# Optimization experiments

Hardware: AMD Instinct MI355X
Metric: run time of the kernel (lower is better)

## Reference

```python
import jax, jax.numpy as jnp
import numpy as np

N_NODES = 100000
N_EDGES = 3200000
D_IN = 256
D_HID = 97


def setup_inputs() -> dict:
    key = jax.random.key(0)
    k1, k2, k3, k4, k5, k6 = jax.random.split(key, 6)
    x = jax.random.normal(k1, (N_NODES, D_IN), dtype=jnp.float32)
    edge_index = jax.random.randint(k2, (2, N_EDGES), 0, N_NODES, dtype=jnp.int64)
    # GCNConv weights (stored as [in, out]) and biases
    W1 = jax.random.normal(k3, (D_IN, D_HID), dtype=jnp.float32) / np.sqrt(D_IN)
    b1 = jnp.zeros((D_HID,), dtype=jnp.float32)
    W2 = jax.random.normal(k4, (D_HID, D_HID), dtype=jnp.float32) / np.sqrt(D_HID)
    b2 = jnp.zeros((D_HID,), dtype=jnp.float32)
    return {"x": x, "edge_index": edge_index, "W1": W1, "b1": b1, "W2": W2, "b2": b2}


def reference(x, edge_index, W1, b1, W2, b2):
    # PyG GCNConv: add self-loops, symmetric degree normalization,
    # out[i] = sum_j norm_ij * (x[j] @ W) + b
    N = x.shape[0]
    self_idx = jnp.arange(N, dtype=edge_index.dtype)
    src = jnp.concatenate([edge_index[0], self_idx])  # source j
    dst = jnp.concatenate([edge_index[1], self_idx])  # target i
    deg = jax.ops.segment_sum(jnp.ones_like(dst, dtype=x.dtype), dst, num_segments=N)
    dinv = jnp.where(deg > 0, 1.0 / jnp.sqrt(deg), 0.0)
    norm = dinv[src] * dinv[dst]  # [E+N]

    def gcn(h, W, b):
        h = h @ W  # dense linear transform first (out_dim small)
        msg = h[src] * norm[:, None]  # gather + scale
        agg = jax.ops.segment_sum(msg, dst, num_segments=N)  # scatter-add
        return agg + b

    h = jax.nn.relu(gcn(x, W1, b1))
    out = gcn(h, W2, b2)
    return out
```

## Files before the change

kernel.cpp:

```cpp
#include <hip/hip_runtime.h>
#include <hip/hip_fp16.h>
#include <stdint.h>

#define D_IN 256
#define D_H  97
#define RST  96
#define NPB  512
#define NBMAX 256
#define CHUNK 4096

typedef _Float16 f16;
typedef f16   f16x8 __attribute__((ext_vector_type(8)));
typedef float f32x4 __attribute__((ext_vector_type(4)));

__device__ __forceinline__ int load_idx(const void* p, int is64, long long pos) {
  if (is64) return (int)(((const long long*)p)[pos]);
  return ((const int*)p)[pos];
}

__global__ __launch_bounds__(256) void detect_prep(
    const void* ei, long long E, int* flag, int* __restrict__ bcur, int nbuck,
    const float* __restrict__ W1, const float* __restrict__ b1,
    const float* __restrict__ W2, const float* __restrict__ b2,
    f16* __restrict__ W1lin, f16* __restrict__ W2lin,
    float* __restrict__ b1p, float* __restrict__ b2p) {
  int tid = threadIdx.x;
  if (blockIdx.x == 0) {
    const int* p32 = (const int*)ei;
    long long stride = E / 1024; if (stride < 1) stride = 1;
    for (int i = tid; i <= nbuck; i += 256) bcur[i] = 0;
    int bad = 0;
    for (int s = 0; s < 4; ++s) {
      long long k = ((long long)tid * 4 + s) * stride;
      if (k < E) {
        if (p32[2 * k + 1] != 0) bad = 1;
      }
    }
    __shared__ int sh_bad;
    if (tid == 0) sh_bad = 0;
    __syncthreads();
    if (bad) atomicOr(&sh_bad, 1);
    __syncthreads();
    if (tid == 0) *flag = sh_bad ? 0 : 1;
    return;
  }
  int idx = (blockIdx.x - 1) * 256 + tid;
  const int n1 = 8 * 7 * 512;
  const int n2 = 4 * 7 * 512;
  if (idx < n1) {
    int fid = idx >> 3, hh = idx & 7;
    int lane = fid & 63, fg = fid >> 6;
    int kb = fg / 7, cg = fg % 7;
    int c = cg * 16 + (lane & 15);
    int k = kb * 32 + (lane >> 4) * 8 + hh;
    W1lin[idx] = (f16)((c < D_H && k < 256) ? W1[k * D_H + c] : 0.f);
  } else if (idx < n1 + n2) {
    int j = idx - n1;
    int fid = j >> 3, hh = j & 7;
    int lane = fid & 63, fg = fid >> 6;
    int kb = fg / 7, cg = fg % 7;
    int c = cg * 16 + (lane & 15);
    int k = kb * 32 + (lane >> 4) * 8 + hh;
    W2lin[j] = (f16)((c < D_H && k < D_H) ? W2[k * D_H + c] : 0.f);
  } else if (idx < n1 + n2 + 128) {
    int c = idx - (n1 + n2);
    b1p[c] = (c < D_H) ? b1[c] : 0.0f;
  } else if (idx < n1 + n2 + 256) {
    int c = idx - (n1 + n2 + 128);
    b2p[c] = (c < D_H) ? b2[c] : 0.0f;
  }
}

template<int KI, bool IN_HALF, bool SCALE_DINV>
__device__ __forceinline__ void gemm_body(
    int gb, const float* __restrict__ Af, const f16* __restrict__ Ah,
    const __half2* __restrict__ sideA,
    const f16* __restrict__ Wlin, const float* __restrict__ dinv,
    f16* __restrict__ C, __half2* __restrict__ sideC, int N) {
  int tid = threadIdx.x, wave = tid >> 6, lane = tid & 63;
  int row0 = gb * 128;
  int m = lane & 15, q = lane >> 4;
  int kf = q * 8;
  int r0 = row0 + wave * 32 + m;
  int r1 = r0 + 16;
  int rr0 = (r0 < N) ? r0 : 0;
  int rr1 = (r1 < N) ? r1 : 0;
  const f16* wbase = Wlin + lane * 8;

  f16x8 a0[KI], a1[KI];
  #pragma unroll
  for (int kb = 0; kb < KI; ++kb) {
    if constexpr (!IN_HALF) {
      const float* p0 = &Af[(size_t)rr0 * 256 + kb * 32 + kf];
      const float* p1 = &Af[(size_t)rr1 * 256 + kb * 32 + kf];
      float4 u0 = *(const float4*)p0, u1 = *(const float4*)(p0 + 4);
      float4 w0 = *(const float4*)p1, w1 = *(const float4*)(p1 + 4);
      f16x8 t0, t1;
      t0[0] = (f16)u0.x; t0[1] = (f16)u0.y; t0[2] = (f16)u0.z; t0[3] = (f16)u0.w;
      t0[4] = (f16)u1.x; t0[5] = (f16)u1.y; t0[6] = (f16)u1.z; t0[7] = (f16)u1.w;
      t1[0] = (f16)w0.x; t1[1] = (f16)w0.y; t1[2] = (f16)w0.z; t1[3] = (f16)w0.w;
      t1[4] = (f16)w1.x; t1[5] = (f16)w1.y; t1[6] = (f16)w1.z; t1[7] = (f16)w1.w;
      a0[kb] = t0; a1[kb] = t1;
    } else {
      if (kb < KI - 1) {
        a0[kb] = *(const f16x8*)&Ah[(size_t)rr0 * RST + kb * 32 + kf];
        a1[kb] = *(const f16x8*)&Ah[(size_t)rr1 * RST + kb * 32 + kf];
      } else {
        f16x8 z0, z1;
        #pragma unroll
        for (int j = 0; j < 8; ++j) { z0[j] = (f16)0.f; z1[j] = (f16)0.f; }
        if (q == 0) {
          z0[0] = ((const f16*)sideA)[2 * rr0];
          z1[0] = ((const f16*)sideA)[2 * rr1];
        }
        a0[kb] = z0; a1[kb] = z1;
      }
    }
  }

  f32x4 acc[2][7];
  #pragma unroll
  for (int mg = 0; mg < 2; ++mg)
    #pragma unroll
    for (int cg = 0; cg < 7; ++cg)
      #pragma unroll
      for (int j = 0; j < 4; ++j) acc[mg][cg][j] = 0.f;

  #pragma unroll
  for (int kb = 0; kb < KI; ++kb) {
    #pragma unroll
    for (int cg = 0; cg < 7; ++cg) {
      f16x8 b = *(const f16x8*)&wbase[(kb * 7 + cg) * 512];
      acc[0][cg] = __builtin_amdgcn_mfma_f32_16x16x32_f16(a0[kb], b, acc[0][cg], 0, 0, 0);
      acc[1][cg] = __builtin_amdgcn_mfma_f32_16x16x32_f16(a1[kb], b, acc[1][cg], 0, 0, 0);
    }
  }

  int colb = m, rq = q * 4;
  #pragma unroll
  for (int mg = 0; mg < 2; ++mg) {
    #pragma unroll
    for (int j = 0; j < 4; ++j) {
      int r = row0 + wave * 32 + mg * 16 + rq + j;
      if (r >= N) continue;
      float dv = SCALE_DINV ? dinv[r] : 1.0f;
      #pragma unroll
      for (int cg = 0; cg < 7; ++cg) {
        int c = cg * 16 + colb;
        float val = SCALE_DINV ? (acc[mg][cg][j] * dv) : acc[mg][cg][j];
        if (c < 96)       C[(size_t)r * RST + c] = (f16)val;
        else if (c == 96) sideC[r] = __floats2half2_rn(val, 0.f);
      }
    }
  }
}

__global__ __launch_bounds__(256) void scatter_gemm1(
    const void* ei, const int* __restrict__ flag, int* __restrict__ bcur,
    unsigned int* __restrict__ bsd, long long E, int nbuck, int cap, int nScat,
    const float* __restrict__ x, const f16* __restrict__ W1lin,
    f16* __restrict__ t1, __half2* __restrict__ sideT, int N) {
  __shared__ unsigned int packs[CHUNK];
  __shared__ unsigned char bkts[CHUNK];
  __shared__ int hist[NBMAX];
  __shared__ int gpos[NBMAX];
  __shared__ int cur[NBMAX];
  int tid = threadIdx.x;
  if ((int)blockIdx.x >= nScat) {
    gemm_body<8, false, false>(blockIdx.x - nScat, x, nullptr, nullptr,
                               W1lin, nullptr, t1, sideT, N);
    return;
  }
  if (tid < NBMAX) { hist[tid] = 0; cur[tid] = 0; }
  __syncthreads();
  int f = *flag;
  long long base = (long long)blockIdx.x * CHUNK;
  int cnt = (int)((E - base < CHUNK) ? (E - base) : CHUNK);
  #pragma unroll 4
  for (int i = tid; i < cnt; i += 256) {
    long long e = base + i;
    int s = load_idx(ei, f, e);
    int d = load_idx(ei, f, E + e);
    int b = d >> 9;
    packs[i] = ((unsigned int)(d & (NPB - 1)) << 17) | (unsigned int)s;
    bkts[i] = (unsigned char)b;
    atomicAdd(&hist[b], 1);
  }
  __syncthreads();
  if (tid < nbuck) { int h = hist[tid]; if (h) gpos[tid] = atomicAdd(&bcur[tid], h); }
  __syncthreads();
  #pragma unroll 4
  for (int i = tid; i < cnt; i += 256) {
    int b = bkts[i];
    int r = atomicAdd(&cur[b], 1);
    int idx = gpos[b] + r;
    if (idx < cap) bsd[(size_t)b * cap + idx] = packs[i];
  }
}

__global__ __launch_bounds__(256) void bucket_finalize(
    const unsigned int* __restrict__ bsd, const int* __restrict__ bcur,
    int* __restrict__ row_start, float* __restrict__ dinv,
    int* __restrict__ csr_src, int N, int cap, int nbuck) {
  __shared__ int sc[256];
  __shared__ int h[NPB];
  __shared__ int rs[NPB];
  __shared__ int cur[NPB];
  __shared__ int wsum[4];
  int b = blockIdx.x, tid = threadIdx.x;
  int lane = tid & 63, wid = tid >> 6;
  int v = (tid < nbuck) ? min(bcur[tid], cap) : 0;
  sc[tid] = v;
  h[2 * tid] = 0; h[2 * tid + 1] = 0;
  cur[2 * tid] = 0; cur[2 * tid + 1] = 0;
  __syncthreads();
  for (int o = 1; o < 256; o <<= 1) {
    int a = (tid >= o) ? sc[tid - o] : 0;
    __syncthreads();
    sc[tid] += a;
    __syncthreads();
  }
  int cnt = min(bcur[b], cap);
  int base = sc[b] - cnt;
  if (b == 0 && tid == 0) row_start[N] = sc[255];
  int d0 = b * cap;
  for (int i = tid; i < cnt; i += 256) atomicAdd(&h[bsd[d0 + i] >> 17], 1);
  __syncthreads();
  int a0 = h[2 * tid], a1 = h[2 * tid + 1];
  int tsum = a0 + a1;
  int incl = tsum;
  #pragma unroll
  for (int off = 1; off < 64; off <<= 1) {
    int n = __shfl_up(incl, off, 64);
    if (lane >= off) incl += n;
  }
  if (lane == 63) wsum[wid] = incl;
  __syncthreads();
  int woff = 0;
  for (int k = 0; k < wid; ++k) woff += wsum[k];
  int excl = woff + incl - tsum + base;
  rs[2 * tid] = excl;
  rs[2 * tid + 1] = excl + a0;
  int node0 = b * NPB;
  int n0 = node0 + 2 * tid, n1 = node0 + 2 * tid + 1;
  if (n0 < N) { row_start[n0] = excl;      dinv[n0] = rsqrtf((float)(a0 + 1)); }
  if (n1 < N) { row_start[n1] = excl + a0; dinv[n1] = rsqrtf((float)(a1 + 1)); }
  __syncthreads();
  for (int i = tid; i < cnt; i += 256) {
    unsigned int p = bsd[d0 + i];
    int r = p >> 17;
    int s = (int)(p & 0x1FFFFu);
    int rel = atomicAdd(&cur[r], 1);
    csr_src[rs[r] + rel] = s;
  }
}

__global__ __launch_bounds__(256) void mfma_gemm2(
    const f16* __restrict__ Ah, const __half2* __restrict__ sideA,
    const f16* __restrict__ Wlin, const float* __restrict__ dinv,
    f16* __restrict__ C, __half2* __restrict__ sideC, int N) {
  gemm_body<4, true, true>(blockIdx.x, nullptr, Ah, sideA, Wlin, dinv, C, sideC, N);
}

template<bool OUT_HALF, bool DO_RELU, bool SRC_SCALE>
__global__ __launch_bounds__(256) void agg_kernel(
    const __half* __restrict__ t, const __half2* __restrict__ side,
    const int* __restrict__ csr_src, const int* __restrict__ row_start,
    const float* __restrict__ dinv, const float* __restrict__ bias,
    void* __restrict__ outp, __half2* __restrict__ side_out, int N) {
  int lane = threadIdx.x & 63;
  int node = blockIdx.x * (blockDim.x >> 6) + (threadIdx.x >> 6);
  if (node >= N || lane >= 49) return;
  const char* gbase = (lane < 48) ? (const char*)t + lane * 4 : (const char*)side;
  unsigned gscale = (lane < 48) ? (unsigned)(RST * 2) : 4u;
  auto GATHER = [&](int j) -> float2 {
    return __half22float2(*(const __half2*)(gbase + (size_t)((unsigned)j * gscale)));
  };
  int s = row_start[node], epd = row_start[node + 1];
  float di = dinv[node];
  float2 v = GATHER(node);
  float ax, ay;
  if (SRC_SCALE) { ax = di * v.x; ay = di * v.y; }
  else           { ax = v.x;      ay = v.y; }
  int e = s;
  while ((e & 3) && e < epd) {
    int j = csr_src[e];
    float2 u = GATHER(j);
    if (SRC_SCALE) { float w = dinv[j]; ax = fmaf(w, u.x, ax); ay = fmaf(w, u.y, ay); }
    else           { ax += u.x; ay += u.y; }
    ++e;
  }
  for (; e + 8 <= epd; e += 8) {
    int4 q0 = *(const int4*)(csr_src + e);
    int4 q1 = *(const int4*)(csr_src + e + 4);
    float2 u0 = GATHER(q0.x), u1 = GATHER(q0.y), u2 = GATHER(q0.z), u3 = GATHER(q0.w);
    float2 u4 = GATHER(q1.x), u5 = GATHER(q1.y), u6 = GATHER(q1.z), u7 = GATHER(q1.w);
    if (SRC_SCALE) {
      float w0 = dinv[q0.x], w1 = dinv[q0.y], w2 = dinv[q0.z], w3 = dinv[q0.w];
      float w4 = dinv[q1.x], w5 = dinv[q1.y], w6 = dinv[q1.z], w7 = dinv[q1.w];
      ax += (fmaf(w0, u0.x, w1 * u1.x) + fmaf(w2, u2.x, w3 * u3.x)) +
            (fmaf(w4, u4.x, w5 * u5.x) + fmaf(w6, u6.x, w7 * u7.x));
      ay += (fmaf(w0, u0.y, w1 * u1.y) + fmaf(w2, u2.y, w3 * u3.y)) +
            (fmaf(w4, u4.y, w5 * u5.y) + fmaf(w6, u6.y, w7 * u7.y));
    } else {
      ax += ((u0.x + u1.x) + (u2.x + u3.x)) + ((u4.x + u5.x) + (u6.x + u7.x));
      ay += ((u0.y + u1.y) + (u2.y + u3.y)) + ((u4.y + u5.y) + (u6.y + u7.y));
    }
  }
  if (e + 4 <= epd) {
    int4 q0 = *(const int4*)(csr_src + e);
    float2 u0 = GATHER(q0.x), u1 = GATHER(q0.y), u2 = GATHER(q0.z), u3 = GATHER(q0.w);
    if (SRC_SCALE) {
      float w0 = dinv[q0.x], w1 = dinv[q0.y], w2 = dinv[q0.z], w3 = dinv[q0.w];
      ax += fmaf(w0, u0.x, w1 * u1.x) + fmaf(w2, u2.x, w3 * u3.x);
      ay += fmaf(w0, u0.y, w1 * u1.y) + fmaf(w2, u2.y, w3 * u3.y);
    } else {
      ax += (u0.x + u1.x) + (u2.x + u3.x);
      ay += (u0.y + u1.y) + (u2.y + u3.y);
    }
    e += 4;
  }
  for (; e < epd; ++e) {
    int j = csr_src[e];
    float2 u = GATHER(j);
    if (SRC_SCALE) { float w = dinv[j]; ax = fmaf(w, u.x, ax); ay = fmaf(w, u.y, ay); }
    else           { ax += u.x; ay += u.y; }
  }
  int c0 = 2 * lane;
  ax = ax * di + bias[c0];
  ay = ay * di + bias[c0 + 1];
  if (DO_RELU) { ax = fmaxf(ax, 0.f); ay = fmaxf(ay, 0.f); }
  if (OUT_HALF) {
    if (lane < 48) ((__half2*)((__half*)outp + (size_t)node * RST))[lane] = __floats2half2_rn(ax, ay);
    else           side_out[node] = __floats2half2_rn(ax, 0.f);
  } else {
    float* o = (float*)outp + (size_t)node * D_H;
    if (lane < 48) { o[c0] = ax; o[c0 + 1] = ay; }
    else           o[96] = ax;
  }
}

extern "C" void kernel_launch(void* const* d_in, const int* in_sizes, int n_in,
                              void* d_out, int out_size, void* d_ws, size_t ws_size,
                              hipStream_t stream) {
  const float* x  = (const float*)d_in[0];
  const void*  ei = d_in[1];
  const float* W1 = (const float*)d_in[2];
  const float* b1 = (const float*)d_in[3];
  const float* W2 = (const float*)d_in[4];
  const float* b2 = (const float*)d_in[5];
  int N = in_sizes[0] / D_IN;
  long long E = (long long)in_sizes[1] / 2;
  int nbuck = (N + NPB - 1) / NPB;
  int cap = (int)(E / nbuck) + 8192;

  char* base = (char*)d_ws;
  size_t off = 0;
  auto alloc = [&](size_t bytes) -> void* {
    void* p = base + off;
    off = (off + bytes + 255) & ~(size_t)255;
    return p;
  };
  int*    flag      = (int*)alloc(4);
  float*  dinv      = (float*)alloc((size_t)N * 4);
  int*    row_start = (int*)alloc((size_t)(N + 1) * 4);
  int*    bcur      = (int*)alloc((size_t)(nbuck + 1) * 4);
  int*    csr_src   = (int*)alloc((size_t)E * 4);
  unsigned int* bsd = (unsigned int*)alloc((size_t)nbuck * cap * 4);
  f16*    W1lin     = (f16*)alloc((size_t)8 * 7 * 512 * 2);
  f16*    W2lin     = (f16*)alloc((size_t)4 * 7 * 512 * 2);
  float*  b1p       = (float*)alloc(128 * 4);
  float*  b2p       = (float*)alloc(128 * 4);
  f16*    t1        = (f16*)alloc((size_t)N * RST * 2 + 256);
  __half2* sideT    = (__half2*)alloc((size_t)N * 4 + 256);
  f16*    h1        = (f16*)alloc((size_t)N * RST * 2 + 256);
  __half2* sideH    = (__half2*)alloc((size_t)N * 4 + 256);

  const int prepTot = 8 * 7 * 512 + 4 * 7 * 512 + 256;
  int gPrep = (prepTot + 255) / 256;
  int nScat = (int)((E + CHUNK - 1) / CHUNK);
  int gGemm = (N + 127) / 128;

  detect_prep<<<1 + gPrep, 256, 0, stream>>>(
      ei, E, flag, bcur, nbuck, W1, b1, W2, b2, W1lin, W2lin, b1p, b2p);
  scatter_gemm1<<<nScat + gGemm, 256, 0, stream>>>(
      ei, flag, bcur, bsd, E, nbuck, cap, nScat, x, W1lin, t1, sideT, N);
  bucket_finalize<<<nbuck, 256, 0, stream>>>(
      bsd, bcur, row_start, dinv, csr_src, N, cap, nbuck);
  agg_kernel<true, true, true><<<(N + 3) / 4, 256, 0, stream>>>(
      (const __half*)t1, sideT, csr_src, row_start, dinv, b1p, h1, sideH, N);
  mfma_gemm2<<<gGemm, 256, 0, stream>>>(h1, sideH, W2lin, dinv, t1, sideT, N);
  agg_kernel<false, false, false><<<(N + 3) / 4, 256, 0, stream>>>(
      (const __half*)t1, sideT, csr_src, row_start, dinv, b2p, d_out, nullptr, N);
}
```

Baseline: 352.7 us.

## Pre-scale t1 by dinv in bucket finalize, drop per-edge dinv gathers in agg

The bucket_finalize kernel now scales the layer-1 transformed features t1 and the side column in place by each node's dinv, once it knows the degree. Layer-1 aggregation then just sums neighbour rows and no longer needs a per-edge random gather of dinv[j]. The scatter kernel keeps edge packs in registers instead of shared-memory staging, and the per-row histogram is split into per-wave copies to reduce atomic contention. In exchange, finalize gains an extra read-modify-write pass over t1, and the fp16 values are rounded after scaling.

```diff
diff --git a/kernel.cpp b/kernel.cpp
--- a/kernel.cpp
+++ b/kernel.cpp
@@ -160,8 +160,6 @@
     unsigned int* __restrict__ bsd, long long E, int nbuck, int cap, int nScat,
     const float* __restrict__ x, const f16* __restrict__ W1lin,
     f16* __restrict__ t1, __half2* __restrict__ sideT, int N) {
-  __shared__ unsigned int packs[CHUNK];
-  __shared__ unsigned char bkts[CHUNK];
   __shared__ int hist[NBMAX];
   __shared__ int gpos[NBMAX];
   __shared__ int cur[NBMAX];
@@ -176,33 +174,42 @@
   int f = *flag;
   long long base = (long long)blockIdx.x * CHUNK;
   int cnt = (int)((E - base < CHUNK) ? (E - base) : CHUNK);
-  #pragma unroll 4
-  for (int i = tid; i < cnt; i += 256) {
-    long long e = base + i;
-    int s = load_idx(ei, f, e);
-    int d = load_idx(ei, f, E + e);
-    int b = d >> 9;
-    packs[i] = ((unsigned int)(d & (NPB - 1)) << 17) | (unsigned int)s;
-    bkts[i] = (unsigned char)b;
-    atomicAdd(&hist[b], 1);
+  unsigned int pk[16];
+  int bk[16];
+  #pragma unroll
+  for (int ii = 0; ii < 16; ++ii) {
+    int i = tid + ii * 256;
+    bk[ii] = -1;
+    if (i < cnt) {
+      long long e = base + i;
+      int s = load_idx(ei, f, e);
+      int d = load_idx(ei, f, E + e);
+      int b = d >> 9;
+      pk[ii] = ((unsigned int)(d & (NPB - 1)) << 17) | (unsigned int)s;
+      bk[ii] = b;
+      atomicAdd(&hist[b], 1);
+    }
   }
   __syncthreads();
   if (tid < nbuck) { int h = hist[tid]; if (h) gpos[tid] = atomicAdd(&bcur[tid], h); }
   __syncthreads();
-  #pragma unroll 4
-  for (int i = tid; i < cnt; i += 256) {
-    int b = bkts[i];
-    int r = atomicAdd(&cur[b], 1);
-    int idx = gpos[b] + r;
-    if (idx < cap) bsd[(size_t)b * cap + idx] = packs[i];
+  #pragma unroll
+  for (int ii = 0; ii < 16; ++ii) {
+    if (bk[ii] >= 0) {
+      int r = atomicAdd(&cur[bk[ii]], 1);
+      int idx = gpos[bk[ii]] + r;
+      if (idx < cap) bsd[(size_t)bk[ii] * cap + idx] = pk[ii];
+    }
   }
 }
 
 __global__ __launch_bounds__(256) void bucket_finalize(
     const unsigned int* __restrict__ bsd, const int* __restrict__ bcur,
     int* __restrict__ row_start, float* __restrict__ dinv,
-    int* __restrict__ csr_src, int N, int cap, int nbuck) {
+    int* __restrict__ csr_src, f16* __restrict__ t1, __half2* __restrict__ sideT,
+    int N, int cap, int nbuck) {
   __shared__ int sc[256];
+  __shared__ int hw[4][NPB];
   __shared__ int h[NPB];
   __shared__ int rs[NPB];
   __shared__ int cur[NPB];
@@ -211,7 +218,7 @@
   int lane = tid & 63, wid = tid >> 6;
   int v = (tid < nbuck) ? min(bcur[tid], cap) : 0;
   sc[tid] = v;
-  h[2 * tid] = 0; h[2 * tid + 1] = 0;
+  for (int k = tid; k < 4 * NPB; k += 256) ((int*)hw)[k] = 0;
   cur[2 * tid] = 0; cur[2 * tid + 1] = 0;
   __syncthreads();
   for (int o = 1; o < 256; o <<= 1) {
@@ -224,9 +231,11 @@
   int base = sc[b] - cnt;
   if (b == 0 && tid == 0) row_start[N] = sc[255];
   int d0 = b * cap;
-  for (int i = tid; i < cnt; i += 256) atomicAdd(&h[bsd[d0 + i] >> 17], 1);
-  __syncthreads();
-  int a0 = h[2 * tid], a1 = h[2 * tid + 1];
+  for (int i = tid; i < cnt; i += 256) atomicAdd(&hw[wid][bsd[d0 + i] >> 17], 1);
+  __syncthreads();
+  int a0 = hw[0][2 * tid] + hw[1][2 * tid] + hw[2][2 * tid] + hw[3][2 * tid];
+  int a1 = hw[0][2 * tid + 1] + hw[1][2 * tid + 1] + hw[2][2 * tid + 1] + hw[3][2 * tid + 1];
+  h[2 * tid] = a0; h[2 * tid + 1] = a1;
   int tsum = a0 + a1;
   int incl = tsum;
   #pragma unroll
@@ -253,6 +262,23 @@
     int rel = atomicAdd(&cur[r], 1);
     csr_src[rs[r] + rel] = s;
   }
+  for (int k = tid; k < NPB * 12; k += 256) {
+    int r = k / 12, c8 = (k % 12) * 8;
+    int gr = node0 + r;
+    if (gr >= N) continue;
+    float dv = rsqrtf((float)(h[r] + 1));
+    f16x8 vv = *(f16x8*)&t1[(size_t)gr * RST + c8];
+    #pragma unroll
+    for (int q = 0; q < 8; ++q) vv[q] = (f16)((float)vv[q] * dv);
+    *(f16x8*)&t1[(size_t)gr * RST + c8] = vv;
+  }
+  for (int r = tid; r < NPB; r += 256) {
+    int gr = node0 + r;
+    if (gr >= N) continue;
+    float dv = rsqrtf((float)(h[r] + 1));
+    float sv = __half22float2(sideT[gr]).x;
+    sideT[gr] = __floats2half2_rn(sv * dv, 0.f);
+  }
 }
 
 __global__ __launch_bounds__(256) void mfma_gemm2(
@@ -262,7 +288,7 @@
   gemm_body<4, true, true>(blockIdx.x, nullptr, Ah, sideA, Wlin, dinv, C, sideC, N);
 }
 
-template<bool OUT_HALF, bool DO_RELU, bool SRC_SCALE>
+template<bool OUT_HALF, bool DO_RELU>
 __global__ __launch_bounds__(256) void agg_kernel(
     const __half* __restrict__ t, const __half2* __restrict__ side,
     const int* __restrict__ csr_src, const int* __restrict__ row_start,
@@ -279,52 +305,30 @@
   int s = row_start[node], epd = row_start[node + 1];
   float di = dinv[node];
   float2 v = GATHER(node);
-  float ax, ay;
-  if (SRC_SCALE) { ax = di * v.x; ay = di * v.y; }
-  else           { ax = v.x;      ay = v.y; }
+  float ax = v.x, ay = v.y;
   int e = s;
   while ((e & 3) && e < epd) {
-    int j = csr_src[e];
-    float2 u = GATHER(j);
-    if (SRC_SCALE) { float w = dinv[j]; ax = fmaf(w, u.x, ax); ay = fmaf(w, u.y, ay); }
-    else           { ax += u.x; ay += u.y; }
-    ++e;
+    float2 u = GATHER(csr_src[e]);
+    ax += u.x; ay += u.y; ++e;
   }
   for (; e + 8 <= epd; e += 8) {
     int4 q0 = *(const int4*)(csr_src + e);
     int4 q1 = *(const int4*)(csr_src + e + 4);
     float2 u0 = GATHER(q0.x), u1 = GATHER(q0.y), u2 = GATHER(q0.z), u3 = GATHER(q0.w);
     float2 u4 = GATHER(q1.x), u5 = GATHER(q1.y), u6 = GATHER(q1.z), u7 = GATHER(q1.w);
-    if (SRC_SCALE) {
-      float w0 = dinv[q0.x], w1 = dinv[q0.y], w2 = dinv[q0.z], w3 = dinv[q0.w];
-      float w4 = dinv[q1.x], w5 = dinv[q1.y], w6 = dinv[q1.z], w7 = dinv[q1.w];
-      ax += (fmaf(w0, u0.x, w1 * u1.x) + fmaf(w2, u2.x, w3 * u3.x)) +
-            (fmaf(w4, u4.x, w5 * u5.x) + fmaf(w6, u6.x, w7 * u7.x));
-      ay += (fmaf(w0, u0.y, w1 * u1.y) + fmaf(w2, u2.y, w3 * u3.y)) +
-            (fmaf(w4, u4.y, w5 * u5.y) + fmaf(w6, u6.y, w7 * u7.y));
-    } else {
-      ax += ((u0.x + u1.x) + (u2.x + u3.x)) + ((u4.x + u5.x) + (u6.x + u7.x));
-      ay += ((u0.y + u1.y) + (u2.y + u3.y)) + ((u4.y + u5.y) + (u6.y + u7.y));
-    }
+    ax += ((u0.x + u1.x) + (u2.x + u3.x)) + ((u4.x + u5.x) + (u6.x + u7.x));
+    ay += ((u0.y + u1.y) + (u2.y + u3.y)) + ((u4.y + u5.y) + (u6.y + u7.y));
   }
   if (e + 4 <= epd) {
     int4 q0 = *(const int4*)(csr_src + e);
     float2 u0 = GATHER(q0.x), u1 = GATHER(q0.y), u2 = GATHER(q0.z), u3 = GATHER(q0.w);
-    if (SRC_SCALE) {
-      float w0 = dinv[q0.x], w1 = dinv[q0.y], w2 = dinv[q0.z], w3 = dinv[q0.w];
-      ax += fmaf(w0, u0.x, w1 * u1.x) + fmaf(w2, u2.x, w3 * u3.x);
-      ay += fmaf(w0, u0.y, w1 * u1.y) + fmaf(w2, u2.y, w3 * u3.y);
-    } else {
-      ax += (u0.x + u1.x) + (u2.x + u3.x);
-      ay += (u0.y + u1.y) + (u2.y + u3.y);
-    }
+    ax += (u0.x + u1.x) + (u2.x + u3.x);
+    ay += (u0.y + u1.y) + (u2.y + u3.y);
     e += 4;
   }
   for (; e < epd; ++e) {
-    int j = csr_src[e];
-    float2 u = GATHER(j);
-    if (SRC_SCALE) { float w = dinv[j]; ax = fmaf(w, u.x, ax); ay = fmaf(w, u.y, ay); }
-    else           { ax += u.x; ay += u.y; }
+    float2 u = GATHER(csr_src[e]);
+    ax += u.x; ay += u.y;
   }
   int c0 = 2 * lane;
   ax = ax * di + bias[c0];
@@ -386,10 +390,10 @@
   scatter_gemm1<<<nScat + gGemm, 256, 0, stream>>>(
       ei, flag, bcur, bsd, E, nbuck, cap, nScat, x, W1lin, t1, sideT, N);
   bucket_finalize<<<nbuck, 256, 0, stream>>>(
-      bsd, bcur, row_start, dinv, csr_src, N, cap, nbuck);
-  agg_kernel<true, true, true><<<(N + 3) / 4, 256, 0, stream>>>(
+      bsd, bcur, row_start, dinv, csr_src, t1, sideT, N, cap, nbuck);
+  agg_kernel<true, true><<<(N + 3) / 4, 256, 0, stream>>>(
       (const __half*)t1, sideT, csr_src, row_start, dinv, b1p, h1, sideH, N);
   mfma_gemm2<<<gGemm, 256, 0, stream>>>(h1, sideH, W2lin, dinv, t1, sideT, N);
-  agg_kernel<false, false, false><<<(N + 3) / 4, 256, 0, stream>>>(
+  agg_kernel<false, false><<<(N + 3) / 4, 256, 0, stream>>>(
       (const __half*)t1, sideT, csr_src, row_start, dinv, b2p, d_out, nullptr, N);
 }
```

Result: no change. 357.6 us (+1.4%).
